# Kernel tuning notes

Hardware: AMD Instinct MI355X
Metric: run time of the kernel (lower is better)

## Reference

```python
import jax, jax.numpy as jnp
import numpy as np

# CogForge GroupedQueryAttention (prefill path): GQA + RoPE + sliding-window+global-token mask
B, T, DM = 2, 2048, 768
H, HKV, DH = 12, 4, 64          # d_head = d_model // n_heads
GROUPS = H // HKV               # kv_groups = 3
WIN, GLB = 512, 64              # window_size, global_tokens
THETA = 10000.0


def _rotate_half(x):
    half = x.shape[-1] // 2
    return jnp.concatenate([-x[..., half:], x[..., :half]], axis=-1)


def _rope_cos_sin(seq_len, dim, dtype):
    inv_freq = 1.0 / (THETA ** (jnp.arange(0, dim, 2, dtype=jnp.float32) / dim))
    t = jnp.arange(seq_len, dtype=jnp.float32)
    freqs = jnp.outer(t, inv_freq)                      # [T, DH/2]
    emb = jnp.concatenate([freqs, freqs], axis=-1)      # [T, DH]
    return jnp.cos(emb).astype(dtype)[None, None], jnp.sin(emb).astype(dtype)[None, None]


def _sparse_mask(seq_len):
    # allowed(i,j) = causal AND (within window OR j is a global token)
    i = jnp.arange(seq_len)[:, None]
    j = jnp.arange(seq_len)[None, :]
    allowed = (j <= i) & (((i - j) < WIN) | (j < GLB))
    return jnp.where(allowed, 0.0, -jnp.inf).astype(jnp.float32)  # [T, T]


def setup_inputs() -> dict:
    key = jax.random.key(0)
    kx, kq, kk, kv, ko = jax.random.split(key, 5)
    x = jax.random.normal(kx, (B, T, DM), jnp.float32)
    wq = jax.random.normal(kq, (DM, H * DH), jnp.float32) * 0.02
    wk = jax.random.normal(kk, (DM, HKV * DH), jnp.float32) * 0.02
    wv = jax.random.normal(kv, (DM, HKV * DH), jnp.float32) * 0.02
    wo = jax.random.normal(ko, (H * DH, DM), jnp.float32) * 0.02
    return {"x": x, "wq": wq, "wk": wk, "wv": wv, "wo": wo}


def reference(x, wq, wk, wv, wo):
    # projections -> [B, heads, T, DH]
    q = (x @ wq).reshape(B, T, H, DH).transpose(0, 2, 1, 3)
    k = (x @ wk).reshape(B, T, HKV, DH).transpose(0, 2, 1, 3)
    v = (x @ wv).reshape(B, T, HKV, DH).transpose(0, 2, 1, 3)

    cos, sin = _rope_cos_sin(T, DH, x.dtype)            # [1,1,T,DH]
    q = q * cos + _rotate_half(q) * sin
    k = k * cos + _rotate_half(k) * sin

    # expand kv heads to match query heads (GQA)
    k = jnp.repeat(k, GROUPS, axis=1)                   # [B,H,T,DH]
    v = jnp.repeat(v, GROUPS, axis=1)

    scale = 1.0 / jnp.sqrt(jnp.asarray(DH, x.dtype))
    scores = jnp.einsum('bhtd,bhsd->bhts', q, k) * scale
    scores = scores + _sparse_mask(T)[None, None]
    weights = jax.nn.softmax(scores, axis=-1)           # attn_dropout = 0.0

    out = jnp.einsum('bhts,bhsd->bhtd', weights, v)
    out = out.transpose(0, 2, 1, 3).reshape(B, T, H * DH)
    return out @ wo
```

## Files before the change

### kernel.cpp

```cpp
#include <hip/hip_runtime.h>
#include <hip/hip_bf16.h>


typedef __attribute__((ext_vector_type(8))) short bf16x8;
typedef __attribute__((ext_vector_type(4))) float f32x4;
typedef __attribute__((ext_vector_type(4))) unsigned short u16x4;

#define MFMA __builtin_amdgcn_mfma_f32_16x16x32_bf16

constexpr int BB = 2, TT = 2048, DM = 768, HH = 12, HKV = 4, DH = 64;
constexpr int WIN = 512, GLB = 64;
constexpr float SC2 = 0.18033688011112042f;

__device__ __forceinline__ unsigned short f2b(float f) {
    union { float f; unsigned int u; } v; v.f = f;
    unsigned int r = v.u + 0x7fffu + ((v.u >> 16) & 1u);
    return (unsigned short)(r >> 16);
}

#define GLOAD_LDS(gp, lp)                                                      \
    __builtin_amdgcn_global_load_lds(                                          \
        (const __attribute__((address_space(1))) void*)(gp),                   \
        (__attribute__((address_space(3))) void*)(lp), 16, 0, 0)

__global__ __launch_bounds__(256) void k_prep(const float* __restrict__ x,
                                              unsigned short* __restrict__ xb,
                                              float2* __restrict__ rope) {
    int bid = blockIdx.x, tid = threadIdx.x;
    if (bid < 3072) {
        int i = bid * 256 + tid;
        float4 v = ((const float4*)x)[i];
        u16x4 o; o.x = f2b(v.x); o.y = f2b(v.y); o.z = f2b(v.z); o.w = f2b(v.w);
        ((u16x4*)xb)[i] = o;
    } else {
        int i = (bid - 3072) * 256 + tid;
        int t = i >> 5, p = i & 31;
        float inv = exp2f(-(float)p * (13.287712379549449f / 32.0f));
        float ang = (float)t * inv;
        rope[i] = make_float2(cosf(ang), sinf(ang));
    }
}

__global__ __launch_bounds__(256) void k_tw(const float* __restrict__ wq,
                                            const float* __restrict__ wk,
                                            const float* __restrict__ wv,
                                            const float* __restrict__ wo,
                                            unsigned short* __restrict__ wqT,
                                            unsigned short* __restrict__ wkT,
                                            unsigned short* __restrict__ wvT,
                                            unsigned short* __restrict__ woT) {
    __shared__ float t[32][33];
    int bid = blockIdx.x;
    const float* src; unsigned short* dst; int N, tile;
    if (bid < 576)      { src = wq; dst = wqT; N = 768; tile = bid; }
    else if (bid < 768) { src = wk; dst = wkT; N = 256; tile = bid - 576; }
    else if (bid < 960) { src = wv; dst = wvT; N = 256; tile = bid - 768; }
    else                { src = wo; dst = woT; N = 768; tile = bid - 960; }
    int ntiles = N / 32;
    int k0 = (tile / ntiles) * 32, n0 = (tile % ntiles) * 32;
    int tx = threadIdx.x & 31, ty = threadIdx.x >> 5;
    #pragma unroll
    for (int e = 0; e < 4; ++e) {
        int r = ty + e * 8;
        t[r][tx] = src[(size_t)(k0 + r) * N + n0 + tx];
    }
    __syncthreads();
    #pragma unroll
    for (int e = 0; e < 4; ++e) {
        int r = ty + e * 8;
        dst[(size_t)(n0 + r) * DM + k0 + tx] = f2b(t[tx][r]);
    }
}

__global__ __launch_bounds__(256) void k_qkv(const unsigned short* __restrict__ xb,
                                             const unsigned short* __restrict__ wqT,
                                             const unsigned short* __restrict__ wkT,
                                             const unsigned short* __restrict__ wvT,
                                             unsigned short* __restrict__ qb,
                                             unsigned short* __restrict__ kb,
                                             unsigned short* __restrict__ vtb,
                                             const float2* __restrict__ rope) {
    __shared__ __align__(16) unsigned short Ab[2][128 * 32];
    __shared__ __align__(16) unsigned short Bbuf[2][64 * 32];
    const int tid = threadIdx.x;
    const int wave = tid >> 6, lane = tid & 63;
    const int quad = lane >> 4, col = lane & 15;
    const int y = blockIdx.y;
    int mode, hl;
    const unsigned short* Bt;
    if (y < 12)      { mode = 0; hl = y;      Bt = wqT + (size_t)hl * 64 * DM; }
    else if (y < 16) { mode = 1; hl = y - 12; Bt = wkT + (size_t)hl * 64 * DM; }
    else             { mode = 2; hl = y - 16; Bt = wvT + (size_t)hl * 64 * DM; }
    const int m0b = blockIdx.x * 128;

    const int sr = lane >> 2, sc = (lane & 3) * 8;
    const unsigned short* gA0 = xb + (size_t)(m0b + wave * 32 + sr) * DM + sc;
    const unsigned short* gA1 = gA0 + (size_t)16 * DM;
    const unsigned short* gB  = Bt + (size_t)(wave * 16 + sr) * DM + sc;

    f32x4 acc[2][4];
    #pragma unroll
    for (int rt = 0; rt < 2; ++rt)
        #pragma unroll
        for (int nt = 0; nt < 4; ++nt) acc[rt][nt] = f32x4{0.f, 0.f, 0.f, 0.f};

    GLOAD_LDS(gA0, &Ab[0][wave * 1024]);
    GLOAD_LDS(gA1, &Ab[0][wave * 1024 + 512]);
    GLOAD_LDS(gB,  &Bbuf[0][wave * 512]);
    __syncthreads();

    for (int t = 0; t < 24; ++t) {
        const int buf = t & 1;
        if (t < 23) {
            const int kn = (t + 1) * 32;
            GLOAD_LDS(gA0 + kn, &Ab[buf ^ 1][wave * 1024]);
            GLOAD_LDS(gA1 + kn, &Ab[buf ^ 1][wave * 1024 + 512]);
            GLOAD_LDS(gB + kn,  &Bbuf[buf ^ 1][wave * 512]);
        }
        bf16x8 a0 = *(const bf16x8*)&Ab[buf][(wave * 32 + col) * 32 + quad * 8];
        bf16x8 a1 = *(const bf16x8*)&Ab[buf][(wave * 32 + 16 + col) * 32 + quad * 8];
        __builtin_amdgcn_s_setprio(1);
        #pragma unroll
        for (int nt = 0; nt < 4; ++nt) {
            bf16x8 b = *(const bf16x8*)&Bbuf[buf][(nt * 16 + col) * 32 + quad * 8];
            acc[0][nt] = MFMA(a0, b, acc[0][nt], 0, 0, 0);
            acc[1][nt] = MFMA(a1, b, acc[1][nt], 0, 0, 0);
        }
        __builtin_amdgcn_s_setprio(0);
        __syncthreads();
    }

    if (mode == 2) {
        int b = m0b >> 11;
        #pragma unroll
        for (int nt = 0; nt < 4; ++nt)
            #pragma unroll
            for (int rt = 0; rt < 2; ++rt)
                #pragma unroll
                for (int r = 0; r < 4; ++r) {
                    int m = m0b + wave * 32 + rt * 16 + quad * 4 + r;
                    int t = m & (TT - 1);
                    int d = nt * 16 + col;
                    vtb[((size_t)(b * HKV + hl) * DH + d) * TT + t] = f2b(acc[rt][nt][r]);
                }
        return;
    }
    int nheads = (mode == 0) ? HH : HKV;
    unsigned short* ob = (mode == 0) ? qb : kb;
    #pragma unroll
    for (int rt = 0; rt < 2; ++rt)
        #pragma unroll
        for (int r = 0; r < 4; ++r) {
            int m = m0b + wave * 32 + rt * 16 + quad * 4 + r;
            int t = m & (TT - 1);
            int b = m >> 11;
            float2 cs0 = rope[t * 32 + col];
            float2 cs1 = rope[t * 32 + 16 + col];
            float v0 = acc[rt][0][r], v1 = acc[rt][1][r], v2 = acc[rt][2][r], v3 = acc[rt][3][r];
            unsigned short* dst = ob + ((size_t)(b * nheads + hl) * TT + t) * DH + col;
            dst[0]  = f2b(v0 * cs0.x - v2 * cs0.y);
            dst[16] = f2b(v1 * cs1.x - v3 * cs1.y);
            dst[32] = f2b(v2 * cs0.x + v0 * cs0.y);
            dst[48] = f2b(v3 * cs1.x + v1 * cs1.y);
        }
}

__global__ __launch_bounds__(256) void k_out(const unsigned short* __restrict__ ao,
                                             const unsigned short* __restrict__ woT,
                                             float* __restrict__ out) {
    __shared__ __align__(16) unsigned short Ab[2][128 * 32];
    __shared__ __align__(16) unsigned short Bbuf[2][64 * 32];
    const int tid = threadIdx.x;
    const int wave = tid >> 6, lane = tid & 63;
    const int quad = lane >> 4, col = lane & 15;
    const int m0b = blockIdx.x * 128;
    const int n0 = blockIdx.y * 64;

    const int sr = lane >> 2, sc = (lane & 3) * 8;
    const unsigned short* gA0 = ao + (size_t)(m0b + wave * 32 + sr) * DM + sc;
    const unsigned short* gA1 = gA0 + (size_t)16 * DM;
    const unsigned short* gB  = woT + (size_t)(n0 + wave * 16 + sr) * DM + sc;

    f32x4 acc[2][4];
    #pragma unroll
    for (int rt = 0; rt < 2; ++rt)
        #pragma unroll
        for (int nt = 0; nt < 4; ++nt) acc[rt][nt] = f32x4{0.f, 0.f, 0.f, 0.f};

    GLOAD_LDS(gA0, &Ab[0][wave * 1024]);
    GLOAD_LDS(gA1, &Ab[0][wave * 1024 + 512]);
    GLOAD_LDS(gB,  &Bbuf[0][wave * 512]);
    __syncthreads();

    for (int t = 0; t < 24; ++t) {
        const int buf = t & 1;
        if (t < 23) {
            const int kn = (t + 1) * 32;
            GLOAD_LDS(gA0 + kn, &Ab[buf ^ 1][wave * 1024]);
            GLOAD_LDS(gA1 + kn, &Ab[buf ^ 1][wave * 1024 + 512]);
            GLOAD_LDS(gB + kn,  &Bbuf[buf ^ 1][wave * 512]);
        }
        bf16x8 a0 = *(const bf16x8*)&Ab[buf][(wave * 32 + col) * 32 + quad * 8];
        bf16x8 a1 = *(const bf16x8*)&Ab[buf][(wave * 32 + 16 + col) * 32 + quad * 8];
        __builtin_amdgcn_s_setprio(1);
        #pragma unroll
        for (int nt = 0; nt < 4; ++nt) {
            bf16x8 b = *(const bf16x8*)&Bbuf[buf][(nt * 16 + col) * 32 + quad * 8];
            acc[0][nt] = MFMA(a0, b, acc[0][nt], 0, 0, 0);
            acc[1][nt] = MFMA(a1, b, acc[1][nt], 0, 0, 0);
        }
        __builtin_amdgcn_s_setprio(0);
        __syncthreads();
    }

    #pragma unroll
    for (int rt = 0; rt < 2; ++rt)
        #pragma unroll
        for (int nt = 0; nt < 4; ++nt)
            #pragma unroll
            for (int r = 0; r < 4; ++r) {
                int m = m0b + wave * 32 + rt * 16 + quad * 4 + r;
                out[(size_t)m * DM + n0 + nt * 16 + col] = acc[rt][nt][r];
            }
}

__global__ __launch_bounds__(256) void k_attn(const unsigned short* __restrict__ Q,
                                              const unsigned short* __restrict__ K,
                                              const unsigned short* __restrict__ Vt,
                                              unsigned short* __restrict__ AO) {
    __shared__ __align__(16) unsigned short kbuf[2][64 * 64];
    __shared__ __align__(16) unsigned short vbuf[2][64 * 64];
    const int lane = threadIdx.x & 63;
    const int wave = threadIdx.x >> 6;
    const int quad = lane >> 4, col = lane & 15;
    const int lbid = (blockIdx.x & 7) * 96 + (blockIdx.x >> 3);
    const int qb = lbid & 31, bh = lbid >> 5;
    const int h = bh % HH, b = bh / HH;
    const int hkv = h / 3;
    const int i0 = qb * 64 + wave * 16;
    const int irow = i0 + col;

    const unsigned short* qbase = Q + ((size_t)(b * HH + h) * TT + irow) * DH + quad * 8;
    const bf16x8 qf0 = *(const bf16x8*)qbase;
    const bf16x8 qf1 = *(const bf16x8*)(qbase + 32);
    const unsigned short* kbase = K + (size_t)(b * HKV + hkv) * TT * DH;
    const unsigned short* vbase = Vt + (size_t)(b * HKV + hkv) * DH * TT;

    float m_run = -1e30f, l_lane = 0.f;
    f32x4 accO[4];
    #pragma unroll
    for (int dt = 0; dt < 4; ++dt) accO[dt] = f32x4{0.f, 0.f, 0.f, 0.f};

    int jw0 = (qb * 64 - WIN + 1) & ~63; if (jw0 < 64) jw0 = 64;
    const int jlast = qb * 64;
    const int nt = 1 + ((jlast >= 64) ? (((jlast - jw0) >> 6) + 1) : 0);
    auto j0_of = [&](int t) { return (t == 0) ? 0 : (jw0 + ((t - 1) << 6)); };

    const int srow = wave * 16 + (lane >> 3);
    const int sq = lane & 7;

    const int L0 = ((((quad * 2) & 3) << 4) | col) << 2;
    const int L1 = ((((quad * 2 + 1) & 3) << 4) | col) << 2;
    const bool hiq = quad >= 2;

    uint4 g0, g1, g2, g3;
    auto stage_load = [&](int j0) {
        const unsigned short* ks = kbase + (size_t)(j0 + srow) * DH + sq * 8;
        const unsigned short* vs = vbase + (size_t)srow * TT + j0 + sq * 8;
        g0 = *(const uint4*)ks;
        g1 = *(const uint4*)(ks + 8 * DH);
        g2 = *(const uint4*)vs;
        g3 = *(const uint4*)(vs + 8 * TT);
    };
    auto stage_write = [&](int bb) {
        unsigned short* kd = &kbuf[bb][srow * 64 + sq * 8];
        unsigned short* vd = &vbuf[bb][srow * 64 + sq * 8];
        *(uint4*)kd = g0;
        *(uint4*)(kd + 8 * 64) = g1;
        *(uint4*)vd = g2;
        *(uint4*)(vd + 8 * 64) = g3;
    };

    stage_load(0);
    stage_write(0);
    __syncthreads();

    for (int t = 0; t < nt; ++t) {
        const int bb = t & 1;
        const bool more = (t + 1) < nt;
        if (more) stage_load(j0_of(t + 1));

        const int j0 = j0_of(t);
        const int mode = (t == 0) ? ((i0 < 64) ? 1 : 0)
                       : (((j0 + 63 > i0) || (j0 <= i0 + 15 - WIN)) ? 2 : 0);

        f32x4 sT[4];
        #pragma unroll
        for (int f = 0; f < 4; ++f) sT[f] = f32x4{0.f, 0.f, 0.f, 0.f};
        __builtin_amdgcn_s_setprio(1);
        #pragma unroll
        for (int f = 0; f < 4; ++f) {
            bf16x8 k0 = *(const bf16x8*)&kbuf[bb][(f * 16 + col) * 64 + quad * 8];
            bf16x8 k1 = *(const bf16x8*)&kbuf[bb][(f * 16 + col) * 64 + 32 + quad * 8];
            sT[f] = MFMA(k0, qf0, sT[f], 0, 0, 0);
            sT[f] = MFMA(k1, qf1, sT[f], 0, 0, 0);
        }
        __builtin_amdgcn_s_setprio(0);

        const int dq = irow - j0 - quad * 4;
        if (mode == 1) {
            #pragma unroll
            for (int f = 0; f < 4; ++f)
                #pragma unroll
                for (int r = 0; r < 4; ++r)
                    if (dq - f * 16 - r < 0) sT[f][r] = -3e30f;
        } else if (mode == 2) {
            #pragma unroll
            for (int f = 0; f < 4; ++f)
                #pragma unroll
                for (int r = 0; r < 4; ++r)
                    if ((unsigned)(dq - f * 16 - r) >= (unsigned)WIN) sT[f][r] = -3e30f;
        }

        float mx = -3e30f;
        #pragma unroll
        for (int f = 0; f < 4; ++f)
            #pragma unroll
            for (int r = 0; r < 4; ++r) mx = fmaxf(mx, sT[f][r]);

        if (!__all(mx <= m_run + 44.f)) {
            float rm = fmaxf(mx, __shfl_xor(mx, 16));
            rm = fmaxf(rm, __shfl_xor(rm, 32));
            float mn = fmaxf(m_run, rm);
            float corr = exp2f((m_run - mn) * SC2);
            m_run = mn;
            l_lane *= corr;
            #pragma unroll
            for (int dt = 0; dt < 4; ++dt)
                #pragma unroll
                for (int r = 0; r < 4; ++r) accO[dt][r] *= corr;
        }

        const float mbase = m_run * SC2;
        unsigned int pk[4][2];
        float ps = 0.f;
        #pragma unroll
        for (int f = 0; f < 4; ++f) {
            float p0 = exp2f(__builtin_fmaf(sT[f][0], SC2, -mbase));
            float p1 = exp2f(__builtin_fmaf(sT[f][1], SC2, -mbase));
            float p2 = exp2f(__builtin_fmaf(sT[f][2], SC2, -mbase));
            float p3 = exp2f(__builtin_fmaf(sT[f][3], SC2, -mbase));
            ps += (p0 + p1) + (p2 + p3);
            asm("v_cvt_pk_bf16_f32 %0, %1, %2" : "=v"(pk[f][0]) : "v"(p0), "v"(p1));
            asm("v_cvt_pk_bf16_f32 %0, %1, %2" : "=v"(pk[f][1]) : "v"(p2), "v"(p3));
        }
        l_lane += ps;

        bf16x8 vf[8];
        #pragma unroll
        for (int js = 0; js < 2; ++js)
            #pragma unroll
            for (int dt = 0; dt < 4; ++dt)
                vf[js * 4 + dt] =
                    *(const bf16x8*)&vbuf[bb][(dt * 16 + col) * 64 + js * 32 + quad * 8];

        #pragma unroll
        for (int js = 0; js < 2; ++js) {
            int fa = 2 * js, fb = 2 * js + 1;
            unsigned int a0 = __builtin_amdgcn_ds_bpermute(L0, pk[fa][0]);
            unsigned int a1 = __builtin_amdgcn_ds_bpermute(L0, pk[fa][1]);
            unsigned int a2 = __builtin_amdgcn_ds_bpermute(L1, pk[fa][0]);
            unsigned int a3 = __builtin_amdgcn_ds_bpermute(L1, pk[fa][1]);
            unsigned int b0 = __builtin_amdgcn_ds_bpermute(L0, pk[fb][0]);
            unsigned int b1 = __builtin_amdgcn_ds_bpermute(L0, pk[fb][1]);
            unsigned int b2 = __builtin_amdgcn_ds_bpermute(L1, pk[fb][0]);
            unsigned int b3 = __builtin_amdgcn_ds_bpermute(L1, pk[fb][1]);
            union { bf16x8 v; unsigned int u[4]; } pb;
            pb.u[0] = hiq ? b0 : a0;
            pb.u[1] = hiq ? b1 : a1;
            pb.u[2] = hiq ? b2 : a2;
            pb.u[3] = hiq ? b3 : a3;
            __builtin_amdgcn_s_setprio(1);
            #pragma unroll
            for (int dt = 0; dt < 4; ++dt)
                accO[dt] = MFMA(vf[js * 4 + dt], pb.v, accO[dt], 0, 0, 0);
            __builtin_amdgcn_s_setprio(0);
        }

        if (more) stage_write(bb ^ 1);
        __syncthreads();
    }

    float lr = l_lane;
    lr += __shfl_xor(lr, 16);
    lr += __shfl_xor(lr, 32);
    const float inv = 1.0f / lr;

    unsigned short* dst = AO + ((size_t)b * TT + irow) * DM + h * DH + quad * 4;
    #pragma unroll
    for (int dt = 0; dt < 4; ++dt) {
        u16x4 o;
        o.x = f2b(accO[dt][0] * inv);
        o.y = f2b(accO[dt][1] * inv);
        o.z = f2b(accO[dt][2] * inv);
        o.w = f2b(accO[dt][3] * inv);
        *(u16x4*)(dst + dt * 16) = o;
    }
}

extern "C" void kernel_launch(void* const* d_in, const int* in_sizes, int n_in,
                              void* d_out, int out_size, void* d_ws, size_t ws_size,
                              hipStream_t stream) {
    const float* x  = (const float*)d_in[0];
    const float* wq = (const float*)d_in[1];
    const float* wk = (const float*)d_in[2];
    const float* wv = (const float*)d_in[3];
    const float* wo = (const float*)d_in[4];
    float* out = (float*)d_out;

    char* ws = (char*)d_ws;
    size_t off = 0;
    auto alloc = [&](size_t bytes) -> void* {
        void* p = ws + off;
        off += (bytes + 255) & ~(size_t)255;
        return p;
    };
    const int M = BB * TT;
    unsigned short* xb  = (unsigned short*)alloc((size_t)M * DM * 2);
    unsigned short* wqT = (unsigned short*)alloc((size_t)DM * DM * 2);
    unsigned short* wkT = (unsigned short*)alloc((size_t)(HKV * DH) * DM * 2);
    unsigned short* wvT = (unsigned short*)alloc((size_t)(HKV * DH) * DM * 2);
    unsigned short* woT = (unsigned short*)alloc((size_t)DM * DM * 2);
    unsigned short* qb  = (unsigned short*)alloc((size_t)BB * HH * TT * DH * 2);
    unsigned short* kb  = (unsigned short*)alloc((size_t)BB * HKV * TT * DH * 2);
    unsigned short* vtb = (unsigned short*)alloc((size_t)BB * HKV * DH * TT * 2);
    unsigned short* ao  = (unsigned short*)alloc((size_t)M * DM * 2);
    float2* rope        = (float2*)alloc((size_t)TT * 32 * sizeof(float2));

    k_prep<<<3328, 256, 0, stream>>>(x, xb, rope);
    k_tw<<<1536, 256, 0, stream>>>(wq, wk, wv, wo, wqT, wkT, wvT, woT);
    k_qkv<<<dim3(M / 128, 20), 256, 0, stream>>>(xb, wqT, wkT, wvT, qb, kb, vtb, rope);
    k_attn<<<768, 256, 0, stream>>>(qb, kb, vtb, ao);
    k_out<<<dim3(M / 128, 12), 256, 0, stream>>>(ao, woT, out);
}
```

Before: 75.33 us.

## Merge prep kernels, widen GEMM K-tile with XOR-swizzled LDS, swizzle attention K/V

After: 61.36 us. 18.6% less time.

```diff
diff --git a/kernel.cpp b/kernel.cpp
--- a/kernel.cpp
+++ b/kernel.cpp
@@ -23,42 +23,43 @@
         (const __attribute__((address_space(1))) void*)(gp),                   \
         (__attribute__((address_space(3))) void*)(lp), 16, 0, 0)
 
-__global__ __launch_bounds__(256) void k_prep(const float* __restrict__ x,
-                                              unsigned short* __restrict__ xb,
-                                              float2* __restrict__ rope) {
+__global__ __launch_bounds__(256) void k_pre(const float* __restrict__ x,
+                                             unsigned short* __restrict__ xb,
+                                             float2* __restrict__ rope,
+                                             const float* __restrict__ wq,
+                                             const float* __restrict__ wk,
+                                             const float* __restrict__ wv,
+                                             const float* __restrict__ wo,
+                                             unsigned short* __restrict__ wqT,
+                                             unsigned short* __restrict__ wkT,
+                                             unsigned short* __restrict__ wvT,
+                                             unsigned short* __restrict__ woT) {
+    __shared__ float t[32][33];
     int bid = blockIdx.x, tid = threadIdx.x;
     if (bid < 3072) {
         int i = bid * 256 + tid;
         float4 v = ((const float4*)x)[i];
         u16x4 o; o.x = f2b(v.x); o.y = f2b(v.y); o.z = f2b(v.z); o.w = f2b(v.w);
         ((u16x4*)xb)[i] = o;
-    } else {
+        return;
+    }
+    if (bid < 3328) {
         int i = (bid - 3072) * 256 + tid;
-        int t = i >> 5, p = i & 31;
+        int tt = i >> 5, p = i & 31;
         float inv = exp2f(-(float)p * (13.287712379549449f / 32.0f));
-        float ang = (float)t * inv;
+        float ang = (float)tt * inv;
         rope[i] = make_float2(cosf(ang), sinf(ang));
-    }
-}
-
-__global__ __launch_bounds__(256) void k_tw(const float* __restrict__ wq,
-                                            const float* __restrict__ wk,
-                                            const float* __restrict__ wv,
-                                            const float* __restrict__ wo,
-                                            unsigned short* __restrict__ wqT,
-                                            unsigned short* __restrict__ wkT,
-                                            unsigned short* __restrict__ wvT,
-                                            unsigned short* __restrict__ woT) {
-    __shared__ float t[32][33];
-    int bid = blockIdx.x;
+        return;
+    }
+    int wb = bid - 3328;
     const float* src; unsigned short* dst; int N, tile;
-    if (bid < 576)      { src = wq; dst = wqT; N = 768; tile = bid; }
-    else if (bid < 768) { src = wk; dst = wkT; N = 256; tile = bid - 576; }
-    else if (bid < 960) { src = wv; dst = wvT; N = 256; tile = bid - 768; }
-    else                { src = wo; dst = woT; N = 768; tile = bid - 960; }
+    if (wb < 576)      { src = wq; dst = wqT; N = 768; tile = wb; }
+    else if (wb < 768) { src = wk; dst = wkT; N = 256; tile = wb - 576; }
+    else if (wb < 960) { src = wv; dst = wvT; N = 256; tile = wb - 768; }
+    else               { src = wo; dst = woT; N = 768; tile = wb - 960; }
     int ntiles = N / 32;
     int k0 = (tile / ntiles) * 32, n0 = (tile % ntiles) * 32;
-    int tx = threadIdx.x & 31, ty = threadIdx.x >> 5;
+    int tx = tid & 31, ty = tid >> 5;
     #pragma unroll
     for (int e = 0; e < 4; ++e) {
         int r = ty + e * 8;
@@ -80,8 +81,8 @@
                                              unsigned short* __restrict__ kb,
                                              unsigned short* __restrict__ vtb,
                                              const float2* __restrict__ rope) {
-    __shared__ __align__(16) unsigned short Ab[2][128 * 32];
-    __shared__ __align__(16) unsigned short Bbuf[2][64 * 32];
+    __shared__ __align__(16) unsigned short Ab[2][128 * 64];
+    __shared__ __align__(16) unsigned short Bb[2][64 * 64];
     const int tid = threadIdx.x;
     const int wave = tid >> 6, lane = tid & 63;
     const int quad = lane >> 4, col = lane & 15;
@@ -93,38 +94,52 @@
     else             { mode = 2; hl = y - 16; Bt = wvT + (size_t)hl * 64 * DM; }
     const int m0b = blockIdx.x * 128;
 
-    const int sr = lane >> 2, sc = (lane & 3) * 8;
-    const unsigned short* gA0 = xb + (size_t)(m0b + wave * 32 + sr) * DM + sc;
-    const unsigned short* gA1 = gA0 + (size_t)16 * DM;
-    const unsigned short* gB  = Bt + (size_t)(wave * 16 + sr) * DM + sc;
+    const int rg = lane >> 3;
+    const int cg = (lane & 7) ^ rg;
+    const int ck = col & 7;
 
     f32x4 acc[2][4];
     #pragma unroll
     for (int rt = 0; rt < 2; ++rt)
         #pragma unroll
-        for (int nt = 0; nt < 4; ++nt) acc[rt][nt] = f32x4{0.f, 0.f, 0.f, 0.f};
-
-    GLOAD_LDS(gA0, &Ab[0][wave * 1024]);
-    GLOAD_LDS(gA1, &Ab[0][wave * 1024 + 512]);
-    GLOAD_LDS(gB,  &Bbuf[0][wave * 512]);
+        for (int j = 0; j < 4; ++j) acc[rt][j] = f32x4{0.f, 0.f, 0.f, 0.f};
+
+    auto stage = [&](int buf, int k) {
+        #pragma unroll
+        for (int m = 0; m < 4; ++m) {
+            int g = wave * 4 + m;
+            GLOAD_LDS(xb + (size_t)(m0b + g * 8 + rg) * DM + k + cg * 8,
+                      &Ab[buf][g * 512]);
+        }
+        #pragma unroll
+        for (int m = 0; m < 2; ++m) {
+            int g = wave * 2 + m;
+            GLOAD_LDS(Bt + (size_t)(g * 8 + rg) * DM + k + cg * 8,
+                      &Bb[buf][g * 512]);
+        }
+    };
+
+    stage(0, 0);
     __syncthreads();
 
-    for (int t = 0; t < 24; ++t) {
+    const int arow0 = (wave * 32 + col) * 64;
+    const int arow1 = (wave * 32 + 16 + col) * 64;
+
+    for (int t = 0; t < 12; ++t) {
         const int buf = t & 1;
-        if (t < 23) {
-            const int kn = (t + 1) * 32;
-            GLOAD_LDS(gA0 + kn, &Ab[buf ^ 1][wave * 1024]);
-            GLOAD_LDS(gA1 + kn, &Ab[buf ^ 1][wave * 1024 + 512]);
-            GLOAD_LDS(gB + kn,  &Bbuf[buf ^ 1][wave * 512]);
-        }
-        bf16x8 a0 = *(const bf16x8*)&Ab[buf][(wave * 32 + col) * 32 + quad * 8];
-        bf16x8 a1 = *(const bf16x8*)&Ab[buf][(wave * 32 + 16 + col) * 32 + quad * 8];
+        if (t < 11) stage(buf ^ 1, (t + 1) * 64);
         __builtin_amdgcn_s_setprio(1);
         #pragma unroll
-        for (int nt = 0; nt < 4; ++nt) {
-            bf16x8 b = *(const bf16x8*)&Bbuf[buf][(nt * 16 + col) * 32 + quad * 8];
-            acc[0][nt] = MFMA(a0, b, acc[0][nt], 0, 0, 0);
-            acc[1][nt] = MFMA(a1, b, acc[1][nt], 0, 0, 0);
+        for (int ks = 0; ks < 2; ++ks) {
+            const int p = ((ks * 4 + quad) ^ ck) * 8;
+            bf16x8 a0 = *(const bf16x8*)&Ab[buf][arow0 + p];
+            bf16x8 a1 = *(const bf16x8*)&Ab[buf][arow1 + p];
+            #pragma unroll
+            for (int j = 0; j < 4; ++j) {
+                bf16x8 b = *(const bf16x8*)&Bb[buf][(j * 16 + col) * 64 + p];
+                acc[0][j] = MFMA(a0, b, acc[0][j], 0, 0, 0);
+                acc[1][j] = MFMA(a1, b, acc[1][j], 0, 0, 0);
+            }
         }
         __builtin_amdgcn_s_setprio(0);
         __syncthreads();
@@ -133,15 +148,15 @@
     if (mode == 2) {
         int b = m0b >> 11;
         #pragma unroll
-        for (int nt = 0; nt < 4; ++nt)
+        for (int j = 0; j < 4; ++j)
             #pragma unroll
             for (int rt = 0; rt < 2; ++rt)
                 #pragma unroll
                 for (int r = 0; r < 4; ++r) {
                     int m = m0b + wave * 32 + rt * 16 + quad * 4 + r;
                     int t = m & (TT - 1);
-                    int d = nt * 16 + col;
-                    vtb[((size_t)(b * HKV + hl) * DH + d) * TT + t] = f2b(acc[rt][nt][r]);
+                    int d = j * 16 + col;
+                    vtb[((size_t)(b * HKV + hl) * DH + d) * TT + t] = f2b(acc[rt][j][r]);
                 }
         return;
     }
@@ -168,46 +183,60 @@
 __global__ __launch_bounds__(256) void k_out(const unsigned short* __restrict__ ao,
                                              const unsigned short* __restrict__ woT,
                                              float* __restrict__ out) {
-    __shared__ __align__(16) unsigned short Ab[2][128 * 32];
-    __shared__ __align__(16) unsigned short Bbuf[2][64 * 32];
+    __shared__ __align__(16) unsigned short Ab[2][128 * 64];
+    __shared__ __align__(16) unsigned short Bb[2][64 * 64];
     const int tid = threadIdx.x;
     const int wave = tid >> 6, lane = tid & 63;
     const int quad = lane >> 4, col = lane & 15;
     const int m0b = blockIdx.x * 128;
     const int n0 = blockIdx.y * 64;
 
-    const int sr = lane >> 2, sc = (lane & 3) * 8;
-    const unsigned short* gA0 = ao + (size_t)(m0b + wave * 32 + sr) * DM + sc;
-    const unsigned short* gA1 = gA0 + (size_t)16 * DM;
-    const unsigned short* gB  = woT + (size_t)(n0 + wave * 16 + sr) * DM + sc;
+    const int rg = lane >> 3;
+    const int cg = (lane & 7) ^ rg;
+    const int ck = col & 7;
 
     f32x4 acc[2][4];
     #pragma unroll
     for (int rt = 0; rt < 2; ++rt)
         #pragma unroll
-        for (int nt = 0; nt < 4; ++nt) acc[rt][nt] = f32x4{0.f, 0.f, 0.f, 0.f};
-
-    GLOAD_LDS(gA0, &Ab[0][wave * 1024]);
-    GLOAD_LDS(gA1, &Ab[0][wave * 1024 + 512]);
-    GLOAD_LDS(gB,  &Bbuf[0][wave * 512]);
+        for (int j = 0; j < 4; ++j) acc[rt][j] = f32x4{0.f, 0.f, 0.f, 0.f};
+
+    auto stage = [&](int buf, int k) {
+        #pragma unroll
+        for (int m = 0; m < 4; ++m) {
+            int g = wave * 4 + m;
+            GLOAD_LDS(ao + (size_t)(m0b + g * 8 + rg) * DM + k + cg * 8,
+                      &Ab[buf][g * 512]);
+        }
+        #pragma unroll
+        for (int m = 0; m < 2; ++m) {
+            int g = wave * 2 + m;
+            GLOAD_LDS(woT + (size_t)(n0 + g * 8 + rg) * DM + k + cg * 8,
+                      &Bb[buf][g * 512]);
+        }
+    };
+
+    stage(0, 0);
     __syncthreads();
 
-    for (int t = 0; t < 24; ++t) {
+    const int arow0 = (wave * 32 + col) * 64;
+    const int arow1 = (wave * 32 + 16 + col) * 64;
+
+    for (int t = 0; t < 12; ++t) {
         const int buf = t & 1;
-        if (t < 23) {
-            const int kn = (t + 1) * 32;
-            GLOAD_LDS(gA0 + kn, &Ab[buf ^ 1][wave * 1024]);
-            GLOAD_LDS(gA1 + kn, &Ab[buf ^ 1][wave * 1024 + 512]);
-            GLOAD_LDS(gB + kn,  &Bbuf[buf ^ 1][wave * 512]);
-        }
-        bf16x8 a0 = *(const bf16x8*)&Ab[buf][(wave * 32 + col) * 32 + quad * 8];
-        bf16x8 a1 = *(const bf16x8*)&Ab[buf][(wave * 32 + 16 + col) * 32 + quad * 8];
+        if (t < 11) stage(buf ^ 1, (t + 1) * 64);
         __builtin_amdgcn_s_setprio(1);
         #pragma unroll
-        for (int nt = 0; nt < 4; ++nt) {
-            bf16x8 b = *(const bf16x8*)&Bbuf[buf][(nt * 16 + col) * 32 + quad * 8];
-            acc[0][nt] = MFMA(a0, b, acc[0][nt], 0, 0, 0);
-            acc[1][nt] = MFMA(a1, b, acc[1][nt], 0, 0, 0);
+        for (int ks = 0; ks < 2; ++ks) {
+            const int p = ((ks * 4 + quad) ^ ck) * 8;
+            bf16x8 a0 = *(const bf16x8*)&Ab[buf][arow0 + p];
+            bf16x8 a1 = *(const bf16x8*)&Ab[buf][arow1 + p];
+            #pragma unroll
+            for (int j = 0; j < 4; ++j) {
+                bf16x8 b = *(const bf16x8*)&Bb[buf][(j * 16 + col) * 64 + p];
+                acc[0][j] = MFMA(a0, b, acc[0][j], 0, 0, 0);
+                acc[1][j] = MFMA(a1, b, acc[1][j], 0, 0, 0);
+            }
         }
         __builtin_amdgcn_s_setprio(0);
         __syncthreads();
@@ -216,11 +245,11 @@
     #pragma unroll
     for (int rt = 0; rt < 2; ++rt)
         #pragma unroll
-        for (int nt = 0; nt < 4; ++nt)
+        for (int j = 0; j < 4; ++j)
             #pragma unroll
             for (int r = 0; r < 4; ++r) {
                 int m = m0b + wave * 32 + rt * 16 + quad * 4 + r;
-                out[(size_t)m * DM + n0 + nt * 16 + col] = acc[rt][nt][r];
+                out[(size_t)m * DM + n0 + j * 16 + col] = acc[rt][j][r];
             }
 }
 
@@ -257,7 +286,9 @@
     auto j0_of = [&](int t) { return (t == 0) ? 0 : (jw0 + ((t - 1) << 6)); };
 
     const int srow = wave * 16 + (lane >> 3);
-    const int sq = lane & 7;
+    const int sk = (lane >> 3) & 7;
+    const int sq = (lane & 7) ^ sk;
+    const int ck = col & 7;
 
     const int L0 = ((((quad * 2) & 3) << 4) | col) << 2;
     const int L1 = ((((quad * 2 + 1) & 3) << 4) | col) << 2;
@@ -273,8 +304,8 @@
         g3 = *(const uint4*)(vs + 8 * TT);
     };
     auto stage_write = [&](int bb) {
-        unsigned short* kd = &kbuf[bb][srow * 64 + sq * 8];
-        unsigned short* vd = &vbuf[bb][srow * 64 + sq * 8];
+        unsigned short* kd = &kbuf[bb][srow * 64 + (lane & 7) * 8];
+        unsigned short* vd = &vbuf[bb][srow * 64 + (lane & 7) * 8];
         *(uint4*)kd = g0;
         *(uint4*)(kd + 8 * 64) = g1;
         *(uint4*)vd = g2;
@@ -300,8 +331,8 @@
         __builtin_amdgcn_s_setprio(1);
         #pragma unroll
         for (int f = 0; f < 4; ++f) {
-            bf16x8 k0 = *(const bf16x8*)&kbuf[bb][(f * 16 + col) * 64 + quad * 8];
-            bf16x8 k1 = *(const bf16x8*)&kbuf[bb][(f * 16 + col) * 64 + 32 + quad * 8];
+            bf16x8 k0 = *(const bf16x8*)&kbuf[bb][(f * 16 + col) * 64 + (quad ^ ck) * 8];
+            bf16x8 k1 = *(const bf16x8*)&kbuf[bb][(f * 16 + col) * 64 + ((4 + quad) ^ ck) * 8];
             sT[f] = MFMA(k0, qf0, sT[f], 0, 0, 0);
             sT[f] = MFMA(k1, qf1, sT[f], 0, 0, 0);
         }
@@ -361,8 +392,8 @@
         for (int js = 0; js < 2; ++js)
             #pragma unroll
             for (int dt = 0; dt < 4; ++dt)
-                vf[js * 4 + dt] =
-                    *(const bf16x8*)&vbuf[bb][(dt * 16 + col) * 64 + js * 32 + quad * 8];
+                vf[js * 4 + dt] = *(const bf16x8*)
+                    &vbuf[bb][(dt * 16 + col) * 64 + ((js * 4 + quad) ^ ck) * 8];
 
         #pragma unroll
         for (int js = 0; js < 2; ++js) {
@@ -437,8 +468,7 @@
     unsigned short* ao  = (unsigned short*)alloc((size_t)M * DM * 2);
     float2* rope        = (float2*)alloc((size_t)TT * 32 * sizeof(float2));
 
-    k_prep<<<3328, 256, 0, stream>>>(x, xb, rope);
-    k_tw<<<1536, 256, 0, stream>>>(wq, wk, wv, wo, wqT, wkT, wvT, woT);
+    k_pre<<<4864, 256, 0, stream>>>(x, xb, rope, wq, wk, wv, wo, wqT, wkT, wvT, woT);
     k_qkv<<<dim3(M / 128, 20), 256, 0, stream>>>(xb, wqT, wkT, wvT, qb, kb, vtb, rope);
     k_attn<<<768, 256, 0, stream>>>(qb, kb, vtb, ao);
     k_out<<<dim3(M / 128, 12), 256, 0, stream>>>(ao, woT, out);
```
